# Optimization experiments

Hardware: AMD Instinct MI355X
Metric: run time of the kernel (lower is better)

## Reference

```python
import jax, jax.numpy as jnp
import numpy as np

D = 1024
H = 16
HD = D // H
FF = 4 * D

def layer_norm(x, g, b, eps=1e-5):
    mu = jnp.mean(x, axis=-1, keepdims=True)
    var = jnp.var(x, axis=-1, keepdims=True)
    return (x - mu) * jax.lax.rsqrt(var + eps) * g + b

def setup_inputs() -> dict:
    key = jax.random.key(0)
    ks = jax.random.split(key, 8)
    s = 0.02
    return {
        "x": jax.random.normal(ks[0], (2, 2048, D), jnp.float32),
        "ln1_g": jnp.ones((D,), jnp.float32),
        "ln1_b": jnp.zeros((D,), jnp.float32),
        "w_qkv": jax.random.normal(ks[1], (3 * D, D), jnp.float32) * s,
        "b_qkv": jnp.zeros((3 * D,), jnp.float32),
        "w_proj": jax.random.normal(ks[2], (D, D), jnp.float32) * s,
        "b_proj": jnp.zeros((D,), jnp.float32),
        "ln2_g": jnp.ones((D,), jnp.float32),
        "ln2_b": jnp.zeros((D,), jnp.float32),
        "w_fc1": jax.random.normal(ks[3], (FF, D), jnp.float32) * s,
        "b_fc1": jnp.zeros((FF,), jnp.float32),
        "w_fc2": jax.random.normal(ks[4], (D, FF), jnp.float32) * s,
        "b_fc2": jnp.zeros((D,), jnp.float32),
    }

def reference(x, ln1_g, ln1_b, w_qkv, b_qkv, w_proj, b_proj,
              ln2_g, ln2_b, w_fc1, b_fc1, w_fc2, b_fc2):
    B, N, C = x.shape
    scale = HD ** -0.5
    # --- attention branch (pre-norm) ---
    h = layer_norm(x, ln1_g, ln1_b)
    qkv = h @ w_qkv.T + b_qkv                      # [B,N,3D]
    qkv = qkv.reshape(B, N, 3, H, HD).transpose(2, 0, 3, 1, 4)
    q, k, v = qkv[0], qkv[1], qkv[2]               # [B,H,N,HD]
    attn = jnp.einsum('bhnd,bhmd->bhnm', q, k) * scale
    attn = jax.nn.softmax(attn, axis=-1)
    o = jnp.einsum('bhnm,bhmd->bhnd', attn, v)     # [B,H,N,HD]
    o = o.transpose(0, 2, 1, 3).reshape(B, N, C)
    x = x + (o @ w_proj.T + b_proj)
    # --- FFN branch (pre-norm) ---
    h = layer_norm(x, ln2_g, ln2_b)
    h = jax.nn.gelu(h @ w_fc1.T + b_fc1, approximate=False)
    x = x + (h @ w_fc2.T + b_fc2)
    return x
```

## Files before the change

kernel.cpp:

```cpp
#include <hip/hip_runtime.h>

typedef __attribute__((ext_vector_type(8))) short short8;
typedef __attribute__((ext_vector_type(4))) float f32x4;

static __device__ __forceinline__ unsigned short f2bf(float f){
  unsigned u = __float_as_uint(f);
  u += 0x7FFF + ((u >> 16) & 1);
  return (unsigned short)(u >> 16);
}

static __device__ __forceinline__ f32x4 MF(short8 a, short8 b, f32x4 c){
  return __builtin_amdgcn_mfma_f32_16x16x32_bf16(a, b, c, 0, 0, 0);
}

#define GL16(g, l) __builtin_amdgcn_global_load_lds( \
    (const __attribute__((address_space(1))) void*)(g), \
    (__attribute__((address_space(3))) void*)(l), 16, 0, 0)

#define SBAR { __builtin_amdgcn_sched_barrier(0); __builtin_amdgcn_s_barrier(); __builtin_amdgcn_sched_barrier(0); }

__global__ __launch_bounds__(256) void cvt_all(
    const float* __restrict__ a0, const float* __restrict__ a1,
    const float* __restrict__ a2, const float* __restrict__ a3,
    unsigned short* __restrict__ o0, unsigned short* __restrict__ o1,
    unsigned short* __restrict__ o2, unsigned short* __restrict__ o3){
  int i = blockIdx.x * 256 + threadIdx.x;
  const float* src; unsigned short* dst; int off;
  if (i < 786432)       { src = a0; dst = o0; off = i; }
  else if (i < 1048576) { src = a1; dst = o1; off = i - 786432; }
  else if (i < 2097152) { src = a2; dst = o2; off = i - 1048576; }
  else                  { src = a3; dst = o3; off = i - 2097152; }
  float4 v = reinterpret_cast<const float4*>(src)[off];
  ushort4 o;
  o.x = f2bf(v.x); o.y = f2bf(v.y); o.z = f2bf(v.z); o.w = f2bf(v.w);
  reinterpret_cast<ushort4*>(dst)[off] = o;
}

__global__ __launch_bounds__(256) void ln_bf16(const float* __restrict__ x,
    const float* __restrict__ g, const float* __restrict__ b,
    unsigned short* __restrict__ out){
  int row = blockIdx.x, t = threadIdx.x;
  const float* xr = x + (size_t)row * 1024;
  float4 xv = reinterpret_cast<const float4*>(xr)[t];
  float s  = xv.x + xv.y + xv.z + xv.w;
  float sq = xv.x*xv.x + xv.y*xv.y + xv.z*xv.z + xv.w*xv.w;
  #pragma unroll
  for (int m = 32; m >= 1; m >>= 1){ s += __shfl_xor(s, m); sq += __shfl_xor(sq, m); }
  __shared__ float ss[4], ssq[4];
  int w = t >> 6, lane = t & 63;
  if (lane == 0){ ss[w] = s; ssq[w] = sq; }
  __syncthreads();
  s  = ss[0] + ss[1] + ss[2] + ss[3];
  sq = ssq[0] + ssq[1] + ssq[2] + ssq[3];
  float mu = s * (1.f/1024.f);
  float rs = rsqrtf(sq * (1.f/1024.f) - mu*mu + 1e-5f);
  float4 gv = reinterpret_cast<const float4*>(g)[t];
  float4 bv = reinterpret_cast<const float4*>(b)[t];
  ushort4 o;
  o.x = f2bf((xv.x - mu) * rs * gv.x + bv.x);
  o.y = f2bf((xv.y - mu) * rs * gv.y + bv.y);
  o.z = f2bf((xv.z - mu) * rs * gv.z + bv.z);
  o.w = f2bf((xv.w - mu) * rs * gv.w + bv.w);
  reinterpret_cast<ushort4*>(out + (size_t)row * 1024)[t] = o;
}

template<int EPI>
__global__ __launch_bounds__(512, 2) void gemm8p(
    const unsigned short* __restrict__ A,
    const unsigned short* __restrict__ B,
    const float* __restrict__ bias,
    void* __restrict__ C,
    int M, int N, int K)
{
  __shared__ __attribute__((aligned(16))) short As[2 * 256 * 64];
  __shared__ __attribute__((aligned(16))) short Bs[2 * 256 * 64];
  const int NT = K >> 6;
  int tid = threadIdx.x, lane = tid & 63, wave = tid >> 6;
  int wm = wave >> 2, wn = wave & 3;
  int l15 = lane & 15, hi = lane >> 4;
  int hi2 = hi ^ (((l15 >> 2) & 1) << 1);
  int bm = blockIdx.y * 256, bn = blockIdx.x * 256;
  int lr = lane >> 3;
  int sg8 = ((lane & 7) ^ ((lane >> 5) << 1)) * 8;
  int rb0 = wave * 16;

  f32x4 acc[8][4] = {};
  short8 aR[4][2], bA[2][2], bB[2][2];

  auto stage = [&](int T, int h){
    if (T >= NT) return;
    const unsigned short* src = (h < 2) ? (A + (size_t)(bm + ((h & 1) << 7)) * K)
                                        : (B + (size_t)(bn + ((h & 1) << 7)) * K);
    short* dst = ((h < 2) ? As : Bs) + ((T & 1) << 14) + ((h & 1) << 13);
    const unsigned short* s = src + (size_t)(rb0 + lr) * K + (T << 6) + sg8;
    GL16(s, dst + rb0 * 64);
    GL16(s + (size_t)8 * K, dst + (rb0 + 8) * 64);
  };
  auto LDA = [&](const short* Ab, int m, int kk){
    int R = wm * 128 + m * 16 + l15;
    return *(const short8*)(Ab + R * 64 + kk * 32 + hi2 * 8);
  };
  auto LDB = [&](const short* Bb, int n, int kk){
    int R = wn * 64 + n * 16 + l15;
    return *(const short8*)(Bb + R * 64 + kk * 32 + hi2 * 8);
  };

  stage(0, 0); stage(0, 1); stage(0, 2); stage(0, 3);
  stage(1, 0); stage(1, 1);
  asm volatile("s_waitcnt vmcnt(4)" ::: "memory");
  SBAR;

  for (int i = 0; i < (NT >> 1); ++i){
    int t0 = 2 * i, t1 = t0 + 1;
    const short* A0 = As;            const short* B0 = Bs;
    const short* A1 = As + 16384;    const short* B1 = Bs + 16384;
    #pragma unroll
    for (int m = 0; m < 4; m++){ aR[m][0] = LDA(A0, m, 0); aR[m][1] = LDA(A0, m, 1); }
    #pragma unroll
    for (int n = 0; n < 2; n++){ bA[n][0] = LDB(B0, n, 0); bA[n][1] = LDB(B0, n, 1); }
    __builtin_amdgcn_sched_barrier(0);
    stage(t1, 2);
    SBAR;
    __builtin_amdgcn_s_setprio(1);
    #pragma unroll
    for (int m = 0; m < 4; m++)
      #pragma unroll
      for (int n = 0; n < 2; n++)
        #pragma unroll
        for (int kk = 0; kk < 2; kk++) acc[m][n] = MF(aR[m][kk], bA[n][kk], acc[m][n]);
    __builtin_amdgcn_s_setprio(0);
    SBAR;
    #pragma unroll
    for (int n = 0; n < 2; n++){ bB[n][0] = LDB(B0, n + 2, 0); bB[n][1] = LDB(B0, n + 2, 1); }
    __builtin_amdgcn_sched_barrier(0);
    stage(t1, 3);
    SBAR;
    __builtin_amdgcn_s_setprio(1);
    #pragma unroll
    for (int m = 0; m < 4; m++)
      #pragma unroll
      for (int n = 0; n < 2; n++)
        #pragma unroll
        for (int kk = 0; kk < 2; kk++) acc[m][n + 2] = MF(aR[m][kk], bB[n][kk], acc[m][n + 2]);
    __builtin_amdgcn_s_setprio(0);
    SBAR;
    #pragma unroll
    for (int m = 0; m < 4; m++){ aR[m][0] = LDA(A0, m + 4, 0); aR[m][1] = LDA(A0, m + 4, 1); }
    __builtin_amdgcn_sched_barrier(0);
    stage(t0 + 2, 0);
    SBAR;
    __builtin_amdgcn_s_setprio(1);
    #pragma unroll
    for (int m = 0; m < 4; m++)
      #pragma unroll
      for (int n = 0; n < 2; n++)
        #pragma unroll
        for (int kk = 0; kk < 2; kk++) acc[m + 4][n] = MF(aR[m][kk], bA[n][kk], acc[m + 4][n]);
    __builtin_amdgcn_s_setprio(0);
    SBAR;
    stage(t0 + 2, 1);
    SBAR;
    __builtin_amdgcn_s_setprio(1);
    #pragma unroll
    for (int m = 0; m < 4; m++)
      #pragma unroll
      for (int n = 0; n < 2; n++)
        #pragma unroll
        for (int kk = 0; kk < 2; kk++) acc[m + 4][n + 2] = MF(aR[m][kk], bB[n][kk], acc[m + 4][n + 2]);
    __builtin_amdgcn_s_setprio(0);
    asm volatile("s_waitcnt vmcnt(4)" ::: "memory");
    SBAR;
    #pragma unroll
    for (int m = 0; m < 4; m++){ aR[m][0] = LDA(A1, m, 0); aR[m][1] = LDA(A1, m, 1); }
    #pragma unroll
    for (int n = 0; n < 2; n++){ bA[n][0] = LDB(B1, n, 0); bA[n][1] = LDB(B1, n, 1); }
    __builtin_amdgcn_sched_barrier(0);
    stage(t0 + 2, 2);
    SBAR;
    __builtin_amdgcn_s_setprio(1);
    #pragma unroll
    for (int m = 0; m < 4; m++)
      #pragma unroll
      for (int n = 0; n < 2; n++)
        #pragma unroll
        for (int kk = 0; kk < 2; kk++) acc[m][n] = MF(aR[m][kk], bA[n][kk], acc[m][n]);
    __builtin_amdgcn_s_setprio(0);
    SBAR;
    #pragma unroll
    for (int n = 0; n < 2; n++){ bB[n][0] = LDB(B1, n + 2, 0); bB[n][1] = LDB(B1, n + 2, 1); }
    __builtin_amdgcn_sched_barrier(0);
    stage(t0 + 2, 3);
    SBAR;
    __builtin_amdgcn_s_setprio(1);
    #pragma unroll
    for (int m = 0; m < 4; m++)
      #pragma unroll
      for (int n = 0; n < 2; n++)
        #pragma unroll
        for (int kk = 0; kk < 2; kk++) acc[m][n + 2] = MF(aR[m][kk], bB[n][kk], acc[m][n + 2]);
    __builtin_amdgcn_s_setprio(0);
    SBAR;
    #pragma unroll
    for (int m = 0; m < 4; m++){ aR[m][0] = LDA(A1, m + 4, 0); aR[m][1] = LDA(A1, m + 4, 1); }
    __builtin_amdgcn_sched_barrier(0);
    stage(t0 + 3, 0);
    SBAR;
    __builtin_amdgcn_s_setprio(1);
    #pragma unroll
    for (int m = 0; m < 4; m++)
      #pragma unroll
      for (int n = 0; n < 2; n++)
        #pragma unroll
        for (int kk = 0; kk < 2; kk++) acc[m + 4][n] = MF(aR[m][kk], bA[n][kk], acc[m + 4][n]);
    __builtin_amdgcn_s_setprio(0);
    SBAR;
    stage(t0 + 3, 1);
    SBAR;
    __builtin_amdgcn_s_setprio(1);
    #pragma unroll
    for (int m = 0; m < 4; m++)
      #pragma unroll
      for (int n = 0; n < 2; n++)
        #pragma unroll
        for (int kk = 0; kk < 2; kk++) acc[m + 4][n + 2] = MF(aR[m][kk], bB[n][kk], acc[m + 4][n + 2]);
    __builtin_amdgcn_s_setprio(0);
    asm volatile("s_waitcnt vmcnt(4)" ::: "memory");
    SBAR;
  }

  #pragma unroll
  for (int m = 0; m < 8; m++){
    int row = bm + wm * 128 + m * 16 + hi * 4;
    #pragma unroll
    for (int n = 0; n < 4; n++){
      int col = bn + wn * 64 + n * 16 + l15;
      float bv = bias[col];
      #pragma unroll
      for (int j = 0; j < 4; j++){
        float v = acc[m][n][j] + bv;
        if (EPI == 1){
          float w2 = v * v;
          float t = exp2f(v * fmaf(w2, 0.10294322f, 2.3022078f));
          float r = __builtin_amdgcn_rcpf(1.f + t);
          v = v - v * r;
        }
        ((unsigned short*)C)[(size_t)(row + j) * N + col] = f2bf(v);
      }
    }
  }
}

template<int EPI>
__global__ __launch_bounds__(256) void gemm4w128(
    const unsigned short* __restrict__ A,
    const unsigned short* __restrict__ B,
    const float* __restrict__ bias,
    const float* __restrict__ resid,
    void* __restrict__ C,
    int M, int N, int K)
{
  __shared__ __attribute__((aligned(16))) short As[2][128 * 64];
  __shared__ __attribute__((aligned(16))) short Bs[2][128 * 64];
  const int NT = K >> 6;
  int tid = threadIdx.x, lane = tid & 63, wave = tid >> 6;
  int wm = wave >> 1, wn = wave & 1;
  int l15 = lane & 15, hi = lane >> 4, l7 = l15 & 7;
  int lin = blockIdx.y * 8 + blockIdx.x;
  int xcd = lin & 7, idx = lin >> 3;
  int bm = (xcd * 4 + (idx >> 3)) * 128;
  int bn = (idx & 7) * 128;
  int lr = lane >> 3;
  int sega = ((lane & 7) ^ lr) * 8;
  f32x4 acc[4][4] = {};

  auto stage = [&](int buf, int k0){
    #pragma unroll
    for (int j = 0; j < 4; j++){
      int row = wave * 32 + j * 8;
      GL16(A + (size_t)(bm + row + lr) * K + k0 + sega, &As[buf][row * 64]);
      GL16(B + (size_t)(bn + row + lr) * K + k0 + sega, &Bs[buf][row * 64]);
    }
  };
  auto LDA = [&](int buf, int m, int kk){
    int R = wm * 64 + m * 16 + l15;
    return *(const short8*)(&As[buf][R * 64 + (((kk << 2) | hi) ^ l7) * 8]);
  };
  auto LDB = [&](int buf, int n, int kk){
    int R = wn * 64 + n * 16 + l15;
    return *(const short8*)(&Bs[buf][R * 64 + (((kk << 2) | hi) ^ l7) * 8]);
  };

  stage(0, 0);
  for (int t = 0; t < NT; t++){
    int cur = t & 1;
    if (t + 1 < NT){
      stage(cur ^ 1, (t + 1) << 6);
      asm volatile("s_waitcnt vmcnt(8)" ::: "memory");
    } else {
      asm volatile("s_waitcnt vmcnt(0)" ::: "memory");
    }
    SBAR;
    #pragma unroll
    for (int kk = 0; kk < 2; kk++){
      short8 af[4], bf[4];
      #pragma unroll
      for (int m = 0; m < 4; m++) af[m] = LDA(cur, m, kk);
      #pragma unroll
      for (int n = 0; n < 4; n++) bf[n] = LDB(cur, n, kk);
      __builtin_amdgcn_s_setprio(1);
      #pragma unroll
      for (int m = 0; m < 4; m++)
        #pragma unroll
        for (int n = 0; n < 4; n++)
          acc[m][n] = MF(af[m], bf[n], acc[m][n]);
      __builtin_amdgcn_s_setprio(0);
    }
    SBAR;
  }
  #pragma unroll
  for (int m = 0; m < 4; m++){
    int row = bm + wm * 64 + m * 16 + hi * 4;
    #pragma unroll
    for (int n = 0; n < 4; n++){
      int col = bn + wn * 64 + n * 16 + l15;
      float bv = bias[col];
      #pragma unroll
      for (int j = 0; j < 4; j++){
        float v = acc[m][n][j] + bv;
        int r = row + j;
        if (EPI == 2){
          ((float*)C)[(size_t)r * N + col] = v + resid[(size_t)r * N + col];
        } else {
          ((unsigned short*)C)[(size_t)r * N + col] = f2bf(v);
        }
      }
    }
  }
}

__global__ __launch_bounds__(512) void attn_fwd(const unsigned short* __restrict__ qkv,
                                                unsigned short* __restrict__ o){
  __shared__ __attribute__((aligned(16))) short K_lds[2][64*64];
  __shared__ __attribute__((aligned(16))) short V_lds[2][64*64];
  __shared__ __attribute__((aligned(16))) short P_lds[8][16*64];
  int tid = threadIdx.x, wave = tid >> 6, lane = tid & 63;
  int l15 = lane & 15, hi = lane >> 4, l7 = l15 & 7;
  int bid = blockIdx.x;
  int swz = (bid & 7) * 64 + (bid >> 3);
  int qt = swz & 15, bh = swz >> 4;
  int b = bh >> 4, h = bh & 15;
  const unsigned short* qbase = qkv + (size_t)b * 2048 * 3072 + h * 64;
  const unsigned short* kbase = qbase + 1024;
  const unsigned short* vbase = qbase + 2048;
  int qrow = qt * 128 + wave * 16 + l15;
  short8 qf0 = *(const short8*)(qbase + (size_t)qrow * 3072 + hi * 8);
  short8 qf1 = *(const short8*)(qbase + (size_t)qrow * 3072 + 32 + hi * 8);
  #pragma unroll
  for (int j = 0; j < 8; j++){
    float q0 = __uint_as_float((unsigned)(unsigned short)qf0[j] << 16) * 0.18033688f;
    float q1 = __uint_as_float((unsigned)(unsigned short)qf1[j] << 16) * 0.18033688f;
    qf0[j] = (short)f2bf(q0);
    qf1[j] = (short)f2bf(q1);
  }
  short8 ones8;
  #pragma unroll
  for (int j = 0; j < 8; j++) ones8[j] = (short)0x3F80;
  int vt = tid - 256;
  int ki0 = tid * 2, ki1 = ki0 + 1;
  int kr0 = ki0 >> 3, ks0 = ki0 & 7;
  int kr1 = ki1 >> 3, ks1 = ki1 & 7;
  int kp = vt & 31, ds8 = (vt >> 5) & 7;
  int vcg = kp >> 2, vwi = (2 * kp) & 7;
  f32x4 accO[4] = {};
  f32x4 lacc = {};
  short* Pw = &P_lds[wave][0];

  auto kv_load = [&](int kt, short8& s0, short8& s1){
    if (vt < 0){
      s0 = *(const short8*)(kbase + (size_t)(kt + kr0) * 3072 + ks0 * 8);
      s1 = *(const short8*)(kbase + (size_t)(kt + kr1) * 3072 + ks1 * 8);
    } else {
      const unsigned short* vr = vbase + (size_t)(kt + 2 * kp) * 3072 + ds8 * 8;
      s0 = *(const short8*)vr;
      s1 = *(const short8*)(vr + 3072);
    }
  };
  auto kv_store = [&](int buf, short8 s0, short8 s1){
    if (vt < 0){
      *(short8*)(&K_lds[buf][kr0 * 64 + ((ks0 ^ (kr0 & 7)) << 3)]) = s0;
      *(short8*)(&K_lds[buf][kr1 * 64 + ((ks1 ^ (kr1 & 7)) << 3)]) = s1;
    } else {
      unsigned* Vw = (unsigned*)&V_lds[buf][0];
      #pragma unroll
      for (int j = 0; j < 8; j++){
        int d = ds8 * 8 + j;
        int sa = d * 64 + ((vcg ^ (d & 7)) << 3) + vwi;
        Vw[sa >> 1] = (unsigned)(unsigned short)s0[j] | ((unsigned)(unsigned short)s1[j] << 16);
      }
    }
  };

  {
    short8 s0, s1;
    kv_load(0, s0, s1);
    kv_store(0, s0, s1);
    __syncthreads();
  }

  for (int t = 0; t < 32; t++){
    int cur = t & 1;
    const short* Kc = &K_lds[cur][0];
    const short* Vc = &V_lds[cur][0];
    short8 s0, s1;
    if (t < 31) kv_load((t + 1) * 64, s0, s1);
    f32x4 sacc[4];
    __builtin_amdgcn_s_setprio(1);
    #pragma unroll
    for (int kb = 0; kb < 4; kb++){
      f32x4 s = {};
      short8 ka = *(const short8*)(Kc + (kb * 16 + l15) * 64 + ((hi ^ l7) << 3));
      s = __builtin_amdgcn_mfma_f32_16x16x32_bf16(ka, qf0, s, 0, 0, 0);
      short8 kb_ = *(const short8*)(Kc + (kb * 16 + l15) * 64 + (((4 + hi) ^ l7) << 3));
      s = __builtin_amdgcn_mfma_f32_16x16x32_bf16(kb_, qf1, s, 0, 0, 0);
      sacc[kb] = s;
    }
    __builtin_amdgcn_s_setprio(0);
    unsigned pu[8];
    #pragma unroll
    for (int kb = 0; kb < 4; kb++){
      unsigned u0 = (unsigned)(int)fmaf(sacc[kb][0], 128.f, 16248.6f);
      unsigned u1 = (unsigned)(int)fmaf(sacc[kb][1], 128.f, 16248.6f);
      unsigned u2 = (unsigned)(int)fmaf(sacc[kb][2], 128.f, 16248.6f);
      unsigned u3 = (unsigned)(int)fmaf(sacc[kb][3], 128.f, 16248.6f);
      pu[kb * 2]     = u0 | (u1 << 16);
      pu[kb * 2 + 1] = u2 | (u3 << 16);
    }
    #pragma unroll
    for (int kb = 0; kb < 4; kb++){
      int sa = l15 * 64 + ((((kb << 1) | (hi >> 1)) ^ l7) << 3) + ((hi & 1) << 2);
      *(uint2*)(Pw + sa) = make_uint2(pu[kb * 2], pu[kb * 2 + 1]);
    }
    __builtin_amdgcn_s_setprio(1);
    #pragma unroll
    for (int kb2 = 0; kb2 < 2; kb2++){
      short8 pf = *(const short8*)(Pw + l15 * 64 + ((((kb2 << 2) | hi) ^ l7) << 3));
      #pragma unroll
      for (int db = 0; db < 4; db++){
        short8 vf = *(const short8*)(Vc + (db * 16 + l15) * 64 + ((((kb2 << 2) | hi) ^ l7) << 3));
        accO[db] = __builtin_amdgcn_mfma_f32_16x16x32_bf16(vf, pf, accO[db], 0, 0, 0);
      }
      lacc = __builtin_amdgcn_mfma_f32_16x16x32_bf16(ones8, pf, lacc, 0, 0, 0);
    }
    __builtin_amdgcn_s_setprio(0);
    if (t < 31){
      kv_store(cur ^ 1, s0, s1);
      __syncthreads();
    }
  }
  float inv = 1.f / lacc[0];
  unsigned short* ob = o + (size_t)(b * 2048 + qt * 128 + wave * 16 + l15) * 1024 + h * 64;
  #pragma unroll
  for (int db = 0; db < 4; db++){
    ushort4 w;
    w.x = f2bf(accO[db][0] * inv);
    w.y = f2bf(accO[db][1] * inv);
    w.z = f2bf(accO[db][2] * inv);
    w.w = f2bf(accO[db][3] * inv);
    *(ushort4*)(ob + db * 16 + hi * 4) = w;
  }
}

extern "C" void kernel_launch(void* const* d_in, const int* in_sizes, int n_in,
                              void* d_out, int out_size, void* d_ws, size_t ws_size,
                              hipStream_t stream){
  const float* x      = (const float*)d_in[0];
  const float* ln1_g  = (const float*)d_in[1];
  const float* ln1_b  = (const float*)d_in[2];
  const float* w_qkv  = (const float*)d_in[3];
  const float* b_qkv  = (const float*)d_in[4];
  const float* w_proj = (const float*)d_in[5];
  const float* b_proj = (const float*)d_in[6];
  const float* ln2_g  = (const float*)d_in[7];
  const float* ln2_b  = (const float*)d_in[8];
  const float* w_fc1  = (const float*)d_in[9];
  const float* b_fc1  = (const float*)d_in[10];
  const float* w_fc2  = (const float*)d_in[11];
  const float* b_fc2  = (const float*)d_in[12];
  float* out = (float*)d_out;
  char* ws = (char*)d_ws;
  const size_t MB = 1024 * 1024;
  unsigned short* h     = (unsigned short*)(ws);
  unsigned short* qkv   = (unsigned short*)(ws + 8*MB);
  unsigned short* ob    = (unsigned short*)(ws + 32*MB);
  float*          x1    = (float*)(ws + 40*MB);
  unsigned short* f     = (unsigned short*)(ws + 56*MB);
  unsigned short* wqkvb = (unsigned short*)(ws + 88*MB);
  unsigned short* wprojb= (unsigned short*)(ws + 94*MB);
  unsigned short* wfc1b = (unsigned short*)(ws + 96*MB);
  unsigned short* wfc2b = (unsigned short*)(ws + 104*MB);

  cvt_all<<<12288, 256, 0, stream>>>(w_qkv, w_proj, w_fc1, w_fc2,
                                     wqkvb, wprojb, wfc1b, wfc2b);

  ln_bf16<<<4096, 256, 0, stream>>>(x, ln1_g, ln1_b, h);
  gemm8p<0><<<dim3(12, 16), 512, 0, stream>>>(h, wqkvb, b_qkv, qkv, 4096, 3072, 1024);
  attn_fwd<<<512, 512, 0, stream>>>(qkv, ob);
  gemm4w128<2><<<dim3(8, 32), 256, 0, stream>>>(ob, wprojb, b_proj, x, x1, 4096, 1024, 1024);
  ln_bf16<<<4096, 256, 0, stream>>>(x1, ln2_g, ln2_b, h);
  gemm8p<1><<<dim3(16, 16), 512, 0, stream>>>(h, wfc1b, b_fc1, f, 4096, 4096, 1024);
  gemm4w128<2><<<dim3(8, 32), 256, 0, stream>>>(f, wfc2b, b_fc2, x1, out, 4096, 1024, 4096);
}
```

Measured before the change: 242.9 us.

## Split K across two wave groups in 128x128 GEMM with LDS reduction

Turns the 256-thread 128x128 output GEMM (used for proj and fc2) into a 512-thread kernel where two groups of four waves each handle alternating 64-wide K slices with their own double-buffered LDS tiles. At the end one group writes its partial accumulators to LDS and the other adds them before the bias/residual epilogue. The aim is more waves per CU and more latency hiding for these N=1024 GEMMs, which launch only 256 blocks. The cost is doubled LDS use (64KB), which limits occupancy, plus an extra LDS reduction pass and a block-wide barrier.

```diff
diff --git a/kernel.cpp b/kernel.cpp
--- a/kernel.cpp
+++ b/kernel.cpp
@@ -251,7 +251,7 @@
 }
 
 template<int EPI>
-__global__ __launch_bounds__(256) void gemm4w128(
+__global__ __launch_bounds__(512) void gemm_ks(
     const unsigned short* __restrict__ A,
     const unsigned short* __restrict__ B,
     const float* __restrict__ bias,
@@ -259,11 +259,13 @@
     void* __restrict__ C,
     int M, int N, int K)
 {
-  __shared__ __attribute__((aligned(16))) short As[2][128 * 64];
-  __shared__ __attribute__((aligned(16))) short Bs[2][128 * 64];
-  const int NT = K >> 6;
+  __shared__ __attribute__((aligned(16))) short As[2][2][128 * 64];
+  __shared__ __attribute__((aligned(16))) short Bs[2][2][128 * 64];
+  const int NS = K >> 7;
   int tid = threadIdx.x, lane = tid & 63, wave = tid >> 6;
-  int wm = wave >> 1, wn = wave & 1;
+  int kg = wave >> 2;
+  int ws = wave & 3;
+  int wm = ws >> 1, wn = ws & 1;
   int l15 = lane & 15, hi = lane >> 4, l7 = l15 & 7;
   int lin = blockIdx.y * 8 + blockIdx.x;
   int xcd = lin & 7, idx = lin >> 3;
@@ -276,25 +278,25 @@
   auto stage = [&](int buf, int k0){
     #pragma unroll
     for (int j = 0; j < 4; j++){
-      int row = wave * 32 + j * 8;
-      GL16(A + (size_t)(bm + row + lr) * K + k0 + sega, &As[buf][row * 64]);
-      GL16(B + (size_t)(bn + row + lr) * K + k0 + sega, &Bs[buf][row * 64]);
+      int row = ws * 32 + j * 8;
+      GL16(A + (size_t)(bm + row + lr) * K + k0 + sega, &As[kg][buf][row * 64]);
+      GL16(B + (size_t)(bn + row + lr) * K + k0 + sega, &Bs[kg][buf][row * 64]);
     }
   };
   auto LDA = [&](int buf, int m, int kk){
     int R = wm * 64 + m * 16 + l15;
-    return *(const short8*)(&As[buf][R * 64 + (((kk << 2) | hi) ^ l7) * 8]);
+    return *(const short8*)(&As[kg][buf][R * 64 + (((kk << 2) | hi) ^ l7) * 8]);
   };
   auto LDB = [&](int buf, int n, int kk){
     int R = wn * 64 + n * 16 + l15;
-    return *(const short8*)(&Bs[buf][R * 64 + (((kk << 2) | hi) ^ l7) * 8]);
-  };
-
-  stage(0, 0);
-  for (int t = 0; t < NT; t++){
-    int cur = t & 1;
-    if (t + 1 < NT){
-      stage(cur ^ 1, (t + 1) << 6);
+    return *(const short8*)(&Bs[kg][buf][R * 64 + (((kk << 2) | hi) ^ l7) * 8]);
+  };
+
+  stage(0, kg * 64);
+  for (int j = 0; j < NS; j++){
+    int cur = j & 1;
+    if (j + 1 < NS){
+      stage(cur ^ 1, (j + 1) * 128 + kg * 64);
       asm volatile("s_waitcnt vmcnt(8)" ::: "memory");
     } else {
       asm volatile("s_waitcnt vmcnt(0)" ::: "memory");
@@ -317,21 +319,35 @@
     }
     SBAR;
   }
-  #pragma unroll
-  for (int m = 0; m < 4; m++){
-    int row = bm + wm * 64 + m * 16 + hi * 4;
-    #pragma unroll
-    for (int n = 0; n < 4; n++){
-      int col = bn + wn * 64 + n * 16 + l15;
-      float bv = bias[col];
-      #pragma unroll
-      for (int j = 0; j < 4; j++){
-        float v = acc[m][n][j] + bv;
-        int r = row + j;
-        if (EPI == 2){
-          ((float*)C)[(size_t)r * N + col] = v + resid[(size_t)r * N + col];
-        } else {
-          ((unsigned short*)C)[(size_t)r * N + col] = f2bf(v);
+
+  float* red = (float*)&As[0][0][0];
+  if (kg == 1){
+    #pragma unroll
+    for (int m = 0; m < 4; m++)
+      #pragma unroll
+      for (int n = 0; n < 4; n++)
+        #pragma unroll
+        for (int j = 0; j < 4; j++)
+          red[ws * 4096 + (m * 16 + hi * 4 + j) * 64 + n * 16 + l15] = acc[m][n][j];
+  }
+  __syncthreads();
+  if (kg == 0){
+    #pragma unroll
+    for (int m = 0; m < 4; m++){
+      int row = bm + wm * 64 + m * 16 + hi * 4;
+      #pragma unroll
+      for (int n = 0; n < 4; n++){
+        int col = bn + wn * 64 + n * 16 + l15;
+        float bv = bias[col];
+        #pragma unroll
+        for (int j = 0; j < 4; j++){
+          float v = acc[m][n][j] + red[ws * 4096 + (m * 16 + hi * 4 + j) * 64 + n * 16 + l15] + bv;
+          int r = row + j;
+          if (EPI == 2){
+            ((float*)C)[(size_t)r * N + col] = v + resid[(size_t)r * N + col];
+          } else {
+            ((unsigned short*)C)[(size_t)r * N + col] = f2bf(v);
+          }
         }
       }
     }
@@ -505,8 +521,8 @@
   ln_bf16<<<4096, 256, 0, stream>>>(x, ln1_g, ln1_b, h);
   gemm8p<0><<<dim3(12, 16), 512, 0, stream>>>(h, wqkvb, b_qkv, qkv, 4096, 3072, 1024);
   attn_fwd<<<512, 512, 0, stream>>>(qkv, ob);
-  gemm4w128<2><<<dim3(8, 32), 256, 0, stream>>>(ob, wprojb, b_proj, x, x1, 4096, 1024, 1024);
+  gemm_ks<2><<<dim3(8, 32), 512, 0, stream>>>(ob, wprojb, b_proj, x, x1, 4096, 1024, 1024);
   ln_bf16<<<4096, 256, 0, stream>>>(x1, ln2_g, ln2_b, h);
   gemm8p<1><<<dim3(16, 16), 512, 0, stream>>>(h, wfc1b, b_fc1, f, 4096, 4096, 1024);
-  gemm4w128<2><<<dim3(8, 32), 256, 0, stream>>>(f, wfc2b, b_fc2, x1, out, 4096, 1024, 4096);
-}
+  gemm_ks<2><<<dim3(8, 32), 512, 0, stream>>>(f, wfc2b, b_fc2, x1, out, 4096, 1024, 4096);
+}
```

New measurement: 220.6 us, median of 2. 1.1x faster.
